# Kernel optimization log

Hardware: AMD Instinct MI355X
Metric: run time of the kernel (lower is better)

The kernel has to match this reference:

```python
import jax, jax.numpy as jnp
import numpy as np

EMBED_DIM = 1024
NUM_HEADS = 16
HEAD_DIM = EMBED_DIM // NUM_HEADS
SCALE = HEAD_DIM ** -0.5


def setup_inputs() -> dict:
    key = jax.random.key(0)
    k_x, k_qkv, k_w, k_b = jax.random.split(key, 4)
    B, N = 2, 2048
    x = jax.random.normal(k_x, (B, N, EMBED_DIM), dtype=jnp.float32)
    # nn.Linear weights stored as (out, in); init with small normal
    w_qkv = jax.random.normal(k_qkv, (3 * EMBED_DIM, EMBED_DIM), dtype=jnp.float32) * (EMBED_DIM ** -0.5)
    w_out = jax.random.normal(k_w, (EMBED_DIM, EMBED_DIM), dtype=jnp.float32) * (EMBED_DIM ** -0.5)
    b_out = jax.random.normal(k_b, (EMBED_DIM,), dtype=jnp.float32) * 0.02
    return {"x": x, "w_qkv": w_qkv, "w_out": w_out, "b_out": b_out}


def reference(x, w_qkv, w_out, b_out):
    B, N, _ = x.shape
    # qkv: (B, N, 3*E) -> (B, N, 3, H, Dh)
    qkv = jnp.einsum('bne,fe->bnf', x, w_qkv).reshape(B, N, 3, NUM_HEADS, HEAD_DIM)
    q, k, v = qkv[:, :, 0], qkv[:, :, 1], qkv[:, :, 2]
    scores = jnp.einsum('bnhd,bmhd->bhnm', q, k) * SCALE
    attn = jax.nn.softmax(scores, axis=-1)  # dropout is identity in eval mode
    out = jnp.einsum('bhnm,bmhd->bnhd', attn, v).reshape(B, N, EMBED_DIM)
    return jnp.einsum('bne,fe->bnf', out, w_out) + b_out
```

## Files before the change

kernel.cpp:

```cpp
#include <hip/hip_runtime.h>
#include <stdint.h>
#include <stddef.h>

#define SEQ   2048
#define BATCH 2
#define NTOK  (SEQ*BATCH)
#define EMB   1024
#define QKVN  3072
#define NH    16
#define HD    64

typedef __bf16 bf16x8 __attribute__((ext_vector_type(8)));
typedef float  f32x4  __attribute__((ext_vector_type(4)));

__device__ __forceinline__ unsigned short f2b(float f) {
  union { float f; uint32_t u; } v; v.f = f;
  uint32_t r = v.u + 0x7fffu + ((v.u >> 16) & 1u);
  return (unsigned short)(r >> 16);
}

#define GLOAD_LDS16(gp, lp)                                                    \
  __builtin_amdgcn_global_load_lds(                                            \
      (__attribute__((address_space(1))) void*)(gp),                           \
      (__attribute__((address_space(3))) void*)(lp), 16, 0, 0)

__global__ void cvt3_kernel(const float* __restrict__ x,
                            const float* __restrict__ wq,
                            const float* __restrict__ wo,
                            unsigned short* __restrict__ xb,
                            unsigned short* __restrict__ wqb,
                            unsigned short* __restrict__ wob) {
  int i = blockIdx.x * blockDim.x + threadIdx.x;
  const float* in; unsigned short* out; int k;
  if (i < 1048576)              { in = x;  out = xb;  k = i; }
  else if (i < 1048576+786432)  { in = wq; out = wqb; k = i - 1048576; }
  else                          { in = wo; out = wob; k = i - (1048576+786432); }
  float4 v = ((const float4*)in)[k];
  ushort4 o;
  o.x = f2b(v.x); o.y = f2b(v.y); o.z = f2b(v.z); o.w = f2b(v.w);
  ((ushort4*)out)[k] = o;
}

__global__ __launch_bounds__(256) void gemm_bt(
    const unsigned short* __restrict__ A,
    const unsigned short* __restrict__ B,
    unsigned short* __restrict__ Cb,
    float* __restrict__ Cf,
    const float* __restrict__ bias,
    unsigned short* __restrict__ vt,
    int M, int N, int K, int mode)
{
  __shared__ unsigned short As[128*64];
  __shared__ unsigned short Bs[128*64];

  const int tid  = threadIdx.x;
  const int wave = tid >> 6, lane = tid & 63;
  const int l16  = lane & 15, quad = lane >> 4;
  const int tm = blockIdx.x * 128, tn = blockIdx.y * 128;
  const int wm = (wave & 1) * 64,  wn = (wave >> 1) * 64;

  f32x4 acc[4][4] = {};

  for (int k0 = 0; k0 < K; k0 += 64) {
    __syncthreads();
#pragma unroll
    for (int j = 0; j < 4; ++j) {
      const int p   = (wave*4 + j)*64 + lane;
      const int row = p >> 3;
      const int c   = ((p & 7) ^ (row & 7)) << 3;
      GLOAD_LDS16(A + (size_t)(tm + row)*K + (k0 + c), As + (wave*4 + j)*512);
      GLOAD_LDS16(B + (size_t)(tn + row)*K + (k0 + c), Bs + (wave*4 + j)*512);
    }
    __syncthreads();

#pragma unroll
    for (int ks = 0; ks < 2; ++ks) {
      bf16x8 af[4], bf[4];
#pragma unroll
      for (int i = 0; i < 4; ++i) {
        const int ca = ((ks*4 + quad) ^ (l16 & 7)) << 3;
        af[i] = *(const bf16x8*)(As + (wm + i*16 + l16)*64 + ca);
        bf[i] = *(const bf16x8*)(Bs + (wn + i*16 + l16)*64 + ca);
      }
#pragma unroll
      for (int mi = 0; mi < 4; ++mi)
#pragma unroll
        for (int ni = 0; ni < 4; ++ni)
          acc[mi][ni] = __builtin_amdgcn_mfma_f32_16x16x32_bf16(af[mi], bf[ni], acc[mi][ni], 0, 0, 0);
    }
  }

  if (mode == 1) {
#pragma unroll
    for (int mi = 0; mi < 4; ++mi)
#pragma unroll
      for (int ni = 0; ni < 4; ++ni)
#pragma unroll
        for (int r = 0; r < 4; ++r) {
          const int row = tm + wm + mi*16 + quad*4 + r;
          const int col = tn + wn + ni*16 + l16;
          Cf[(size_t)row*N + col] = acc[mi][ni][r] + bias[col];
        }
  } else {
    if (tn < 2048) {
#pragma unroll
      for (int mi = 0; mi < 4; ++mi)
#pragma unroll
        for (int ni = 0; ni < 4; ++ni)
#pragma unroll
          for (int r = 0; r < 4; ++r) {
            const int row = tm + wm + mi*16 + quad*4 + r;
            const int col = tn + wn + ni*16 + l16;
            Cb[(size_t)row*2048 + col] = f2b(acc[mi][ni][r]);
          }
    } else {
#pragma unroll
      for (int mi = 0; mi < 4; ++mi)
#pragma unroll
        for (int ni = 0; ni < 4; ++ni) {
          const int f    = tn + wn + ni*16 + l16 - 2048;
          const int row0 = tm + wm + mi*16 + quad*4;
          const int bb   = row0 >> 11;
          const int n0   = row0 & 2047;
          ushort4 pv;
          pv.x = f2b(acc[mi][ni][0]); pv.y = f2b(acc[mi][ni][1]);
          pv.z = f2b(acc[mi][ni][2]); pv.w = f2b(acc[mi][ni][3]);
          *(ushort4*)(vt + ((size_t)(bb*1024 + f))*2048 + n0) = pv;
        }
    }
  }
}

__global__ __launch_bounds__(256) void attn_kernel(
    const unsigned short* __restrict__ qk,
    const unsigned short* __restrict__ vT,
    unsigned short* __restrict__ aout)
{
  __shared__ unsigned short Ks[4][32*64];
  __shared__ unsigned short Vt[4][64*32];
  __shared__ unsigned short Pl[4*2*16*32];

  const int tid  = threadIdx.x;
  const int wave = tid >> 6, lane = tid & 63;
  const int l16  = lane & 15, quad = lane >> 4;

  const int flat = blockIdx.x;
  const int xcd  = flat & 7;
  const int idx  = flat >> 3;
  const int bh   = xcd*4 + (idx >> 5);
  const int qt   = idx & 31;
  const int b  = bh >> 4, h = bh & 15;
  const size_t tok0 = (size_t)b * SEQ;
  const int qrow0 = qt*64 + wave*16;
  const int ksw = l16 & 7;
  const int xsw = (l16 >> 1) & 3;

  const int p     = wave*64 + lane;
  const int krow  = p >> 3;
  const int kc    = ((p & 7) ^ (krow & 7)) << 3;
  const int vd    = p >> 2;
  const int vc    = ((p & 3) ^ ((vd >> 1) & 3)) << 3;
  const unsigned short* kbase = qk + tok0*2048 + 1024 + h*64;
  const unsigned short* vbase = vT + ((size_t)(b*1024 + h*64))*2048;
  const int ldstw = wave*512;

#define STAGE(bf, t)                                                          \
  do {                                                                        \
    const int _kk = (t)*32;                                                   \
    GLOAD_LDS16(kbase + (size_t)(_kk + krow)*2048 + kc, &Ks[bf][ldstw]);      \
    GLOAD_LDS16(vbase + (size_t)vd*2048 + _kk + vc,     &Vt[bf][ldstw]);      \
  } while (0)

  bf16x8 qf[2];
  {
    const unsigned short* qp = qk + (tok0 + qrow0 + l16)*2048 + h*64;
#pragma unroll
    for (int ks = 0; ks < 2; ++ks) {
      bf16x8 t = *(const bf16x8*)(qp + ks*32 + quad*8);
#pragma unroll
      for (int j = 0; j < 8; ++j) t[j] = (__bf16)((float)t[j] * 0.125f);
      qf[ks] = t;
    }
  }

  f32x4 oacc[4] = {};
  float l_run = 0.f;
  unsigned short* Pw0 = Pl + (wave*2 + 0)*512;
  unsigned short* Pw1 = Pl + (wave*2 + 1)*512;
  const float LOG2E = 1.44269504f;
  const float OFF2  = 17.3123405f;

  STAGE(0, 0);
  STAGE(1, 1);
  __syncthreads();

#pragma unroll 2
  for (int kbb = 0; kbb < SEQ/64; ++kbb) {
    const int t0 = kbb*2;
    const int b0 = t0 & 3, b1 = (t0 + 1) & 3;
    if (t0 + 2 < SEQ/32) { STAGE((t0+2)&3, t0+2); STAGE((t0+3)&3, t0+3); }

    f32x4 sA[2] = {}, sB[2] = {};
    __builtin_amdgcn_s_setprio(1);
#pragma unroll
    for (int ks = 0; ks < 2; ++ks)
#pragma unroll
      for (int mf = 0; mf < 2; ++mf) {
        bf16x8 kf = *(const bf16x8*)(&Ks[b0][(mf*16 + l16)*64 + (((ks*4 + quad) ^ ksw) << 3)]);
        sA[mf] = __builtin_amdgcn_mfma_f32_16x16x32_bf16(kf, qf[ks], sA[mf], 0, 0, 0);
      }
#pragma unroll
    for (int ks = 0; ks < 2; ++ks)
#pragma unroll
      for (int mf = 0; mf < 2; ++mf) {
        bf16x8 kf = *(const bf16x8*)(&Ks[b1][(mf*16 + l16)*64 + (((ks*4 + quad) ^ ksw) << 3)]);
        sB[mf] = __builtin_amdgcn_mfma_f32_16x16x32_bf16(kf, qf[ks], sB[mf], 0, 0, 0);
      }
    __builtin_amdgcn_s_setprio(0);

    {
      float rs = l_run;
#pragma unroll
      for (int mf = 0; mf < 2; ++mf) {
        union { float f; uint32_t u; } a0, a1, a2, a3;
        a0.f = __builtin_amdgcn_exp2f(fmaf(sA[mf][0], LOG2E, -OFF2));
        a1.f = __builtin_amdgcn_exp2f(fmaf(sA[mf][1], LOG2E, -OFF2));
        a2.f = __builtin_amdgcn_exp2f(fmaf(sA[mf][2], LOG2E, -OFF2));
        a3.f = __builtin_amdgcn_exp2f(fmaf(sA[mf][3], LOG2E, -OFF2));
        rs += (a0.f + a1.f) + (a2.f + a3.f);
        uint2 pk;
        pk.x = __builtin_amdgcn_perm(a1.u, a0.u, 0x07060302u);
        pk.y = __builtin_amdgcn_perm(a3.u, a2.u, 0x07060302u);
        *(uint2*)(Pw0 + l16*32 + ((((mf*2 + (quad>>1)) ^ xsw) << 3) + (quad&1)*4)) = pk;
      }
      l_run = rs;
    }
    __builtin_amdgcn_s_setprio(1);
    {
      bf16x8 pf = *(const bf16x8*)(Pw0 + l16*32 + ((quad ^ xsw) << 3));
#pragma unroll
      for (int mf = 0; mf < 4; ++mf) {
        bf16x8 vf = *(const bf16x8*)(&Vt[b0][(mf*16 + l16)*32 + ((quad ^ xsw) << 3)]);
        oacc[mf] = __builtin_amdgcn_mfma_f32_16x16x32_bf16(vf, pf, oacc[mf], 0, 0, 0);
      }
    }
    __builtin_amdgcn_s_setprio(0);

    {
      float rs = l_run;
#pragma unroll
      for (int mf = 0; mf < 2; ++mf) {
        union { float f; uint32_t u; } a0, a1, a2, a3;
        a0.f = __builtin_amdgcn_exp2f(fmaf(sB[mf][0], LOG2E, -OFF2));
        a1.f = __builtin_amdgcn_exp2f(fmaf(sB[mf][1], LOG2E, -OFF2));
        a2.f = __builtin_amdgcn_exp2f(fmaf(sB[mf][2], LOG2E, -OFF2));
        a3.f = __builtin_amdgcn_exp2f(fmaf(sB[mf][3], LOG2E, -OFF2));
        rs += (a0.f + a1.f) + (a2.f + a3.f);
        uint2 pk;
        pk.x = __builtin_amdgcn_perm(a1.u, a0.u, 0x07060302u);
        pk.y = __builtin_amdgcn_perm(a3.u, a2.u, 0x07060302u);
        *(uint2*)(Pw1 + l16*32 + ((((mf*2 + (quad>>1)) ^ xsw) << 3) + (quad&1)*4)) = pk;
      }
      l_run = rs;
    }
    __builtin_amdgcn_s_setprio(1);
    {
      bf16x8 pf = *(const bf16x8*)(Pw1 + l16*32 + ((quad ^ xsw) << 3));
#pragma unroll
      for (int mf = 0; mf < 4; ++mf) {
        bf16x8 vf = *(const bf16x8*)(&Vt[b1][(mf*16 + l16)*32 + ((quad ^ xsw) << 3)]);
        oacc[mf] = __builtin_amdgcn_mfma_f32_16x16x32_bf16(vf, pf, oacc[mf], 0, 0, 0);
      }
    }
    __builtin_amdgcn_s_setprio(0);

    __syncthreads();
  }
#undef STAGE

  {
    float l = l_run;
    l += __shfl_xor(l, 16);
    l += __shfl_xor(l, 32);
    const float inv = 1.0f / l;
    const size_t trow = tok0 + qrow0 + l16;
#pragma unroll
    for (int mf = 0; mf < 4; ++mf) {
      ushort4 ov;
      ov.x = f2b(oacc[mf][0] * inv);
      ov.y = f2b(oacc[mf][1] * inv);
      ov.z = f2b(oacc[mf][2] * inv);
      ov.w = f2b(oacc[mf][3] * inv);
      *(ushort4*)(aout + trow*EMB + h*64 + mf*16 + quad*4) = ov;
    }
  }
}

extern "C" void kernel_launch(void* const* d_in, const int* in_sizes, int n_in,
                              void* d_out, int out_size, void* d_ws, size_t ws_size,
                              hipStream_t stream) {
  const float* x     = (const float*)d_in[0];
  const float* w_qkv = (const float*)d_in[1];
  const float* w_out = (const float*)d_in[2];
  const float* b_out = (const float*)d_in[3];

  char* ws = (char*)d_ws;
  unsigned short* xb    = (unsigned short*)(ws);
  unsigned short* wqkvb = (unsigned short*)(ws + 8388608);
  unsigned short* woutb = (unsigned short*)(ws + 14680064);
  unsigned short* qkb   = (unsigned short*)(ws + 16777216);
  unsigned short* vTb   = (unsigned short*)(ws + 33554432);
  unsigned short* aob   = (unsigned short*)(ws + 41943040);

  cvt3_kernel<<<8192, 256, 0, stream>>>(x, w_qkv, w_out, xb, wqkvb, woutb);

  gemm_bt<<<dim3(NTOK/128, QKVN/128), 256, 0, stream>>>(
      xb, wqkvb, qkb, nullptr, nullptr, vTb, NTOK, QKVN, EMB, 2);

  attn_kernel<<<dim3(1024), 256, 0, stream>>>(qkb, vTb, aob);

  gemm_bt<<<dim3(NTOK/128, EMB/128), 256, 0, stream>>>(
      aob, woutb, nullptr, (float*)d_out, b_out, nullptr, NTOK, EMB, EMB, 1);
}
```

Before: 199.4 us.

## Double-buffer GEMM LDS tiles with a 32-wide K step and prefetch

```diff
diff --git a/kernel.cpp b/kernel.cpp
--- a/kernel.cpp
+++ b/kernel.cpp
@@ -50,8 +50,8 @@
     unsigned short* __restrict__ vt,
     int M, int N, int K, int mode)
 {
-  __shared__ unsigned short As[128*64];
-  __shared__ unsigned short Bs[128*64];
+  __shared__ unsigned short As[2][128*32];
+  __shared__ unsigned short Bs[2][128*32];
 
   const int tid  = threadIdx.x;
   const int wave = tid >> 6, lane = tid & 63;
@@ -59,36 +59,48 @@
   const int tm = blockIdx.x * 128, tn = blockIdx.y * 128;
   const int wm = (wave & 1) * 64,  wn = (wave >> 1) * 64;
 
+  const int e0   = (wave*2 + 0)*512 + lane*8;
+  const int e1   = (wave*2 + 1)*512 + lane*8;
+  const int row0 = e0 >> 5, kk0a = e0 & 31;
+  const int row1 = e1 >> 5, kk1a = e1 & 31;
+  const int ld0  = (wave*2 + 0)*512;
+  const int ld1  = (wave*2 + 1)*512;
+
+#define GSTAGE(bf, k0s)                                                        \
+  do {                                                                         \
+    GLOAD_LDS16(A + (size_t)(tm + row0)*K + ((k0s) + kk0a), As[bf] + ld0);     \
+    GLOAD_LDS16(B + (size_t)(tn + row0)*K + ((k0s) + kk0a), Bs[bf] + ld0);     \
+    GLOAD_LDS16(A + (size_t)(tm + row1)*K + ((k0s) + kk1a), As[bf] + ld1);     \
+    GLOAD_LDS16(B + (size_t)(tn + row1)*K + ((k0s) + kk1a), Bs[bf] + ld1);     \
+  } while (0)
+
   f32x4 acc[4][4] = {};
 
-  for (int k0 = 0; k0 < K; k0 += 64) {
+  GSTAGE(0, 0);
+  __syncthreads();
+
+  int buf = 0;
+  for (int k0 = 0; k0 < K; k0 += 32) {
+    if (k0 + 32 < K) GSTAGE(buf ^ 1, k0 + 32);
+
+    const unsigned short* Ac = As[buf];
+    const unsigned short* Bc = Bs[buf];
+    bf16x8 af[4], bf[4];
+#pragma unroll
+    for (int i = 0; i < 4; ++i) {
+      af[i] = *(const bf16x8*)(Ac + (wm + i*16 + l16)*32 + quad*8);
+      bf[i] = *(const bf16x8*)(Bc + (wn + i*16 + l16)*32 + quad*8);
+    }
+#pragma unroll
+    for (int mi = 0; mi < 4; ++mi)
+#pragma unroll
+      for (int ni = 0; ni < 4; ++ni)
+        acc[mi][ni] = __builtin_amdgcn_mfma_f32_16x16x32_bf16(af[mi], bf[ni], acc[mi][ni], 0, 0, 0);
+
     __syncthreads();
-#pragma unroll
-    for (int j = 0; j < 4; ++j) {
-      const int p   = (wave*4 + j)*64 + lane;
-      const int row = p >> 3;
-      const int c   = ((p & 7) ^ (row & 7)) << 3;
-      GLOAD_LDS16(A + (size_t)(tm + row)*K + (k0 + c), As + (wave*4 + j)*512);
-      GLOAD_LDS16(B + (size_t)(tn + row)*K + (k0 + c), Bs + (wave*4 + j)*512);
-    }
-    __syncthreads();
-
-#pragma unroll
-    for (int ks = 0; ks < 2; ++ks) {
-      bf16x8 af[4], bf[4];
-#pragma unroll
-      for (int i = 0; i < 4; ++i) {
-        const int ca = ((ks*4 + quad) ^ (l16 & 7)) << 3;
-        af[i] = *(const bf16x8*)(As + (wm + i*16 + l16)*64 + ca);
-        bf[i] = *(const bf16x8*)(Bs + (wn + i*16 + l16)*64 + ca);
-      }
-#pragma unroll
-      for (int mi = 0; mi < 4; ++mi)
-#pragma unroll
-        for (int ni = 0; ni < 4; ++ni)
-          acc[mi][ni] = __builtin_amdgcn_mfma_f32_16x16x32_bf16(af[mi], bf[ni], acc[mi][ni], 0, 0, 0);
-    }
-  }
+    buf ^= 1;
+  }
+#undef GSTAGE
 
   if (mode == 1) {
 #pragma unroll
@@ -119,9 +131,9 @@
 #pragma unroll
         for (int ni = 0; ni < 4; ++ni) {
           const int f    = tn + wn + ni*16 + l16 - 2048;
-          const int row0 = tm + wm + mi*16 + quad*4;
-          const int bb   = row0 >> 11;
-          const int n0   = row0 & 2047;
+          const int row0_ = tm + wm + mi*16 + quad*4;
+          const int bb   = row0_ >> 11;
+          const int n0   = row0_ & 2047;
           ushort4 pv;
           pv.x = f2b(acc[mi][ni][0]); pv.y = f2b(acc[mi][ni][1]);
           pv.z = f2b(acc[mi][ni][2]); pv.w = f2b(acc[mi][ni][3]);
```

After: 191.1 us. 4.2% less time.
